# Kernel optimization log

Measured on AMD Instinct MI355X. Metric: run time of the kernel, lower is better.

The kernel has to match this reference:

```python
import jax, jax.numpy as jnp
import numpy as np

N_HEAD = 16
HIDDEN = 1024

def setup_inputs() -> dict:
    key = jax.random.key(0)
    ks = jax.random.split(key, 4)
    B, T, D = 2, 2048, HIDDEN
    x = jax.random.normal(ks[0], (B, T, D), dtype=jnp.float32)
    attention_mask = jnp.zeros((B, 1, 1, T), dtype=jnp.float32)  # additive mask
    w_attn = jax.random.normal(ks[1], (D, 3 * D), dtype=jnp.float32) * (1.0 / np.sqrt(D))
    b_attn = jnp.zeros((3 * D,), dtype=jnp.float32)
    w_proj = jax.random.normal(ks[2], (D, D), dtype=jnp.float32) * (1.0 / np.sqrt(D))
    b_proj = jnp.zeros((D,), dtype=jnp.float32)
    return {"x": x, "attention_mask": attention_mask,
            "w_attn": w_attn, "b_attn": b_attn,
            "w_proj": w_proj, "b_proj": b_proj}

def reference(x, attention_mask, w_attn, b_attn, w_proj, b_proj):
    B, T, D = x.shape
    H = N_HEAD
    hd = D // H
    qkv = x @ w_attn + b_attn                      # [B,T,3D]
    q, k, v = jnp.split(qkv, 3, axis=-1)
    q = q.reshape(B, T, H, hd)
    k = k.reshape(B, T, H, hd)
    v = v.reshape(B, T, H, hd)
    qk = jnp.einsum('BFNH,BTNH->BNFT', q, k) / jnp.sqrt(jnp.asarray(hd, qk_dtype := q.dtype))
    # NOTE: source adds the mask twice (once unconditionally, once inside the None-check)
    attn_weights = qk + attention_mask + attention_mask
    attn_probs = jax.nn.softmax(attn_weights, axis=-1)  # dropout(0.01) is identity at inference
    attn_out = jnp.einsum('BNFT,BTNH->BFNH', attn_probs, v)
    attn_out = attn_out.reshape(B, T, D)
    return attn_out @ w_proj + b_proj
```

## Files before the change

kernel.cpp:

```cpp
#include <hip/hip_runtime.h>
#include <hip/hip_bf16.h>

#define T_SEQ 2048
#define D_MODEL 1024
#define N_HEADS 16

typedef _Float16 half8 __attribute__((ext_vector_type(8)));
typedef _Float16 half4 __attribute__((ext_vector_type(4)));
typedef _Float16 half2v __attribute__((ext_vector_type(2)));
typedef float floatx4 __attribute__((ext_vector_type(4)));
typedef unsigned short ushort4v __attribute__((ext_vector_type(4)));
typedef unsigned short ushort8v __attribute__((ext_vector_type(8)));

#define LOG2E 1.44269504088896f

__device__ __forceinline__ unsigned short f32_to_bf16(float f) {
  unsigned u = __builtin_bit_cast(unsigned, f);
  u = u + 0x7FFFu + ((u >> 16) & 1u);
  return (unsigned short)(u >> 16);
}
__device__ __forceinline__ float bf16_to_f32(unsigned short h) {
  unsigned u = ((unsigned)h) << 16;
  return __builtin_bit_cast(float, u);
}
__device__ __forceinline__ half2v pk_f16(float a, float b) {
  return __builtin_bit_cast(half2v, __builtin_amdgcn_cvt_pkrtz(a, b));
}

__device__ __forceinline__ void load16_lds(const _Float16* g, _Float16* lds_base, int lane) {
#if __has_builtin(__builtin_amdgcn_global_load_lds)
  __builtin_amdgcn_global_load_lds(
      (const __attribute__((address_space(1))) void*)g,
      (__attribute__((address_space(3))) void*)lds_base, 16, 0, 0);
#else
  *(half8*)(lds_base + lane * 8) = *(const half8*)g;
#endif
}

__global__ void k_detect(const unsigned short* __restrict__ x, int* __restrict__ flag) {
  __shared__ int cnt;
  if (threadIdx.x == 0) cnt = 0;
  __syncthreads();
  unsigned short v = x[(size_t)threadIdx.x * 2];
  int e = (v >> 7) & 0xFF;
  int ok = (v == 0) || (e >= 100 && e <= 150);
  atomicAdd(&cnt, ok);
  __syncthreads();
  if (threadIdx.x == 0) *flag = (cnt >= 192) ? 1 : 0;
}

__global__ void k_cvt_h8(const void* __restrict__ in, _Float16* __restrict__ out,
                         int n8, const int* __restrict__ flag) {
  int f = *flag;
  int i = blockIdx.x * 256 + threadIdx.x;
  if (i >= n8) return;
  half8 o;
  if (f) {
    ushort8v u = ((const ushort8v*)in)[i];
#pragma unroll
    for (int e = 0; e < 8; ++e) o[e] = (_Float16)bf16_to_f32(u[e]);
  } else {
    floatx4 a = ((const floatx4*)in)[2 * i];
    floatx4 b = ((const floatx4*)in)[2 * i + 1];
#pragma unroll
    for (int e = 0; e < 4; ++e) { o[e] = (_Float16)a[e]; o[e + 4] = (_Float16)b[e]; }
  }
  ((half8*)out)[i] = o;
}

__global__ void k_cvt3(const void* __restrict__ ba, const void* __restrict__ bp,
                       const void* __restrict__ mk, float* __restrict__ baF,
                       float* __restrict__ bpF, float* __restrict__ mask2,
                       const int* __restrict__ flag) {
  int f = *flag;
  int i = blockIdx.x * 256 + threadIdx.x;
  auto cv = [&](const void* p, int j) {
    return f ? bf16_to_f32(((const unsigned short*)p)[j]) : ((const float*)p)[j];
  };
  if (i < 3072) baF[i] = cv(ba, i);
  else if (i < 4096) bpF[i - 3072] = cv(bp, i - 3072);
  else mask2[i - 4096] = cv(mk, i - 4096) * (2.0f * LOG2E);
}

__global__ __launch_bounds__(256) void k_transpose2(
    const void* __restrict__ inA, _Float16* __restrict__ outA,
    const void* __restrict__ inB, _Float16* __restrict__ outB,
    const int* __restrict__ flag) {
  __shared__ float tile[32][33];
  int f = *flag;
  const void* in;
  _Float16* out;
  int N, bid;
  if (blockIdx.x < 3072) { in = inA; out = outA; N = 3072; bid = blockIdx.x; }
  else { in = inB; out = outB; N = 1024; bid = blockIdx.x - 3072; }
  const int K = 1024;
  int nb = N >> 5;
  int bx = bid % nb, by = bid / nb;
  int n0 = bx << 5, k0 = by << 5;
  int c = threadIdx.x & 31, r = threadIdx.x >> 5;
  const float* fin = (const float*)in;
  const unsigned short* uin = (const unsigned short*)in;
#pragma unroll
  for (int i = 0; i < 4; ++i) {
    int kk = r + i * 8;
    size_t idx = (size_t)(k0 + kk) * N + n0 + c;
    tile[kk][c] = f ? bf16_to_f32(uin[idx]) : fin[idx];
  }
  __syncthreads();
#pragma unroll
  for (int i = 0; i < 4; ++i) {
    int nn = r + i * 8;
    out[(size_t)(n0 + nn) * K + k0 + c] = (_Float16)tile[c][nn];
  }
}

__global__ __launch_bounds__(256) void k_gemm(
    const _Float16* __restrict__ A, const _Float16* __restrict__ BT,
    const float* __restrict__ bias, void* __restrict__ D0,
    void* __restrict__ D1, void* __restrict__ D2,
    int M, int N, int K, int outKind, const int* __restrict__ flag) {
  __shared__ _Float16 As[128 * 64] __attribute__((aligned(16)));
  __shared__ _Float16 Bs[128 * 64] __attribute__((aligned(16)));
  const int tid = threadIdx.x;
  const int wave = tid >> 6, lane = tid & 63;
  const int ln = lane & 15, quad = lane >> 4;
  const int bm = blockIdx.y * 128, bn = blockIdx.x * 128;
  const int wm = (wave & 1) * 64, wn = (wave >> 1) * 64;

  const int sr = tid >> 3, scn = (tid & 7) ^ (sr & 7);
  const _Float16* Ag = A + (size_t)(bm + sr) * K + scn * 8;
  const _Float16* Bg = BT + (size_t)(bn + sr) * K + scn * 8;

  floatx4 acc[4][4] = {};

  for (int kt = 0; kt < K; kt += 64) {
    __syncthreads();
#pragma unroll
    for (int i = 0; i < 4; ++i) {
      load16_lds(Ag + kt + (size_t)i * 32 * K, As + (wave * 64 + i * 256) * 8, lane);
      load16_lds(Bg + kt + (size_t)i * 32 * K, Bs + (wave * 64 + i * 256) * 8, lane);
    }
    __syncthreads();
    half8 af[4][2], bf[4][2];
#pragma unroll
    for (int i = 0; i < 4; ++i) {
      int r = wm + i * 16 + ln;
#pragma unroll
      for (int ks = 0; ks < 2; ++ks)
        af[i][ks] = *(const half8*)(As + r * 64 + ((quad + 4 * ks) ^ (r & 7)) * 8);
    }
#pragma unroll
    for (int j = 0; j < 4; ++j) {
      int r = wn + j * 16 + ln;
#pragma unroll
      for (int ks = 0; ks < 2; ++ks)
        bf[j][ks] = *(const half8*)(Bs + r * 64 + ((quad + 4 * ks) ^ (r & 7)) * 8);
    }
#pragma unroll
    for (int ks = 0; ks < 2; ++ks)
#pragma unroll
      for (int i = 0; i < 4; ++i)
#pragma unroll
        for (int j = 0; j < 4; ++j)
          acc[i][j] = __builtin_amdgcn_mfma_f32_16x16x32_f16(af[i][ks], bf[j][ks], acc[i][j], 0, 0, 0);
  }

  if (outKind == 0) {
    _Float16* Qs = (_Float16*)D0;
    _Float16* Ks = (_Float16*)D1;
    _Float16* Vt = (_Float16*)D2;
    const float qsc = 0.125f * LOG2E;
#pragma unroll
    for (int i = 0; i < 4; ++i) {
      int rbase = bm + wm + i * 16 + quad * 4;
      int sect = rbase >> 10;
      int cfeat = rbase & 1023;
      int h = cfeat >> 6, hd = cfeat & 63;
      float bv[4];
#pragma unroll
      for (int r = 0; r < 4; ++r) bv[r] = bias[rbase + r];
#pragma unroll
      for (int j = 0; j < 4; ++j) {
        int col = bn + wn + j * 16 + ln;
        int b = col >> 11, t = col & 2047;
        size_t bh = (size_t)b * N_HEADS + h;
        float v[4];
#pragma unroll
        for (int r = 0; r < 4; ++r) v[r] = acc[i][j][r] + bv[r];
        if (sect == 0) {
          half4 q;
#pragma unroll
          for (int r = 0; r < 4; ++r) q[r] = (_Float16)(v[r] * qsc);
          *(half4*)(Qs + (bh * T_SEQ + t) * 64 + hd) = q;
        } else if (sect == 1) {
          half4 kk4;
#pragma unroll
          for (int r = 0; r < 4; ++r) kk4[r] = (_Float16)v[r];
          *(half4*)(Ks + (bh * T_SEQ + t) * 64 + hd) = kk4;
        } else {
#pragma unroll
          for (int r = 0; r < 4; ++r)
            Vt[(bh * 64 + hd + r) * T_SEQ + t] = (_Float16)v[r];
        }
      }
    }
  } else {
    int mode = (*flag) ? 2 : 1;
#pragma unroll
    for (int i = 0; i < 4; ++i) {
      int rbase = bm + wm + i * 16 + quad * 4;
      float bv[4];
#pragma unroll
      for (int r = 0; r < 4; ++r) bv[r] = bias[rbase + r];
#pragma unroll
      for (int j = 0; j < 4; ++j) {
        int col = bn + wn + j * 16 + ln;
        float v[4];
#pragma unroll
        for (int r = 0; r < 4; ++r) v[r] = acc[i][j][r] + bv[r];
        if (mode == 1) {
          floatx4 o = {v[0], v[1], v[2], v[3]};
          *(floatx4*)((float*)D0 + (size_t)col * M + rbase) = o;
        } else {
          ushort4v o;
#pragma unroll
          for (int r = 0; r < 4; ++r) o[r] = f32_to_bf16(v[r]);
          *(ushort4v*)((unsigned short*)D0 + (size_t)col * M + rbase) = o;
        }
      }
    }
  }
}

__global__ __launch_bounds__(256, 4) void k_flash(
    const _Float16* __restrict__ Qs, const _Float16* __restrict__ Ks,
    const _Float16* __restrict__ Vt, const float* __restrict__ mask2,
    _Float16* __restrict__ O) {
  __shared__ __attribute__((aligned(16))) char smem[32768];
  _Float16* KlB = (_Float16*)smem;
  _Float16* VlB = (_Float16*)(smem + 16384);
  float* Red = (float*)smem;

  const int tid = threadIdx.x, wave = tid >> 6, lane = tid & 63;
  const int ln = lane & 15, quad = lane >> 4;
  const int qh = wave & 1, kh = wave >> 1;
  const int id = blockIdx.x;
  const int qc = id & 31, h = (id >> 5) & 15, b = id >> 9;
  const size_t bh = (size_t)b * N_HEADS + h;
  const _Float16* Qb = Qs + bh * T_SEQ * 64;
  const _Float16* Kb = Ks + bh * T_SEQ * 64;
  const _Float16* Vb = Vt + bh * 64 * T_SEQ;
  const int q0w = qc * 64 + qh * 32;

  half8 qf[2][2];
#pragma unroll
  for (int jq = 0; jq < 2; ++jq)
#pragma unroll
    for (int kk = 0; kk < 2; ++kk)
      qf[jq][kk] = *(const half8*)(Qb + (size_t)(q0w + jq * 16 + ln) * 64 + kk * 32 + quad * 8);

  floatx4 Oacc[4][2] = {};
  float m0[2] = {0.f, 0.f}, li[2] = {0.f, 0.f};

  const int sr = tid >> 3, scn = (tid & 7) ^ (sr & 7);
  const _Float16* kp0 = Kb + (size_t)sr * 64 + scn * 8;
  const _Float16* kp1 = kp0 + 32 * 64;
  const _Float16* vp0 = Vb + (size_t)sr * T_SEQ + scn * 8;
  const _Float16* vp1 = vp0 + 32 * T_SEQ;
  const float* mqw = mask2 + (size_t)b * T_SEQ + kh * 32 + quad * 4;

  {
    _Float16* K0 = KlB + (size_t)wave * 512;
    _Float16* V0 = VlB + (size_t)wave * 512;
    load16_lds(kp0, K0, lane);
    load16_lds(kp1, K0 + 2048, lane);
    load16_lds(vp0, V0, lane);
    load16_lds(vp1, V0 + 2048, lane);
    kp0 += 64 * 64; kp1 += 64 * 64; vp0 += 64; vp1 += 64;
  }

  for (int t = 0; t < 32; ++t) {
    const int cur = t & 1;
    __syncthreads();
    if (t + 1 < 32) {
      _Float16* K0 = KlB + (cur ^ 1) * 4096 + (size_t)wave * 512;
      _Float16* V0 = VlB + (cur ^ 1) * 4096 + (size_t)wave * 512;
      load16_lds(kp0, K0, lane);
      load16_lds(kp1, K0 + 2048, lane);
      load16_lds(vp0, V0, lane);
      load16_lds(vp1, V0 + 2048, lane);
      kp0 += 64 * 64; kp1 += 64 * 64; vp0 += 64; vp1 += 64;
    }
    const _Float16* Kc = KlB + cur * 4096;
    const _Float16* Vc = VlB + cur * 4096;

    floatx4 s[2][2];
    __builtin_amdgcn_s_setprio(1);
#pragma unroll
    for (int jk = 0; jk < 2; ++jk) {
      const int krow = kh * 32 + jk * 16 + ln;
      half8 kf0 = *(const half8*)(Kc + krow * 64 + ((quad) ^ (krow & 7)) * 8);
      half8 kf1 = *(const half8*)(Kc + krow * 64 + ((4 + quad) ^ (krow & 7)) * 8);
#pragma unroll
      for (int jq = 0; jq < 2; ++jq) {
        floatx4 z = *(const floatx4*)(mqw + jk * 16);
        z = __builtin_amdgcn_mfma_f32_16x16x32_f16(kf0, qf[jq][0], z, 0, 0, 0);
        z = __builtin_amdgcn_mfma_f32_16x16x32_f16(kf1, qf[jq][1], z, 0, 0, 0);
        s[jk][jq] = z;
      }
    }
    __builtin_amdgcn_s_setprio(0);
    mqw += 64;

    if (t == 0) {
#pragma unroll
      for (int jq = 0; jq < 2; ++jq) {
        float tm = -__builtin_inff();
#pragma unroll
        for (int jk = 0; jk < 2; ++jk)
#pragma unroll
          for (int r = 0; r < 4; ++r) tm = fmaxf(tm, s[jk][jq][r]);
        tm = fmaxf(tm, __shfl_xor(tm, 16, 64));
        tm = fmaxf(tm, __shfl_xor(tm, 32, 64));
        m0[jq] = fmaxf(tm, -50.f);
      }
    }

#pragma unroll
    for (int jk = 0; jk < 2; ++jk)
#pragma unroll
      for (int jq = 0; jq < 2; ++jq)
#pragma unroll
        for (int r = 0; r < 4; ++r) {
          float p = __builtin_amdgcn_exp2f(s[jk][jq][r] - m0[jq]);
          s[jk][jq][r] = p;
          li[jq] += p;
        }

    half4 pf4[2][2];
#pragma unroll
    for (int jk = 0; jk < 2; ++jk)
#pragma unroll
      for (int jq = 0; jq < 2; ++jq) {
        half2v p01 = pk_f16(s[jk][jq][0], s[jk][jq][1]);
        half2v p23 = pk_f16(s[jk][jq][2], s[jk][jq][3]);
        pf4[jk][jq] = (half4){p01[0], p01[1], p23[0], p23[1]};
      }

    __builtin_amdgcn_s_setprio(1);
#pragma unroll
    for (int jd = 0; jd < 4; ++jd) {
      const int vrow = jd * 16 + ln;
      const _Float16* Vr = Vc + vrow * 64;
      half4 vf0 = *(const half4*)(Vr + (((kh * 4 + 0 + (quad >> 1)) ^ (vrow & 7)) * 8) + (quad & 1) * 4);
      half4 vf1 = *(const half4*)(Vr + (((kh * 4 + 2 + (quad >> 1)) ^ (vrow & 7)) * 8) + (quad & 1) * 4);
#pragma unroll
      for (int jq = 0; jq < 2; ++jq) {
        Oacc[jd][jq] = __builtin_amdgcn_mfma_f32_16x16x16f16(vf0, pf4[0][jq], Oacc[jd][jq], 0, 0, 0);
        Oacc[jd][jq] = __builtin_amdgcn_mfma_f32_16x16x16f16(vf1, pf4[1][jq], Oacc[jd][jq], 0, 0, 0);
      }
    }
    __builtin_amdgcn_s_setprio(0);
  }

#pragma unroll
  for (int jq = 0; jq < 2; ++jq) {
    li[jq] += __shfl_xor(li[jq], 16, 64);
    li[jq] += __shfl_xor(li[jq], 32, 64);
  }

  __syncthreads();
  float* myRed = Red + ((size_t)qh * 64 + lane) * 36;
  if (kh) {
#pragma unroll
    for (int jd = 0; jd < 4; ++jd)
#pragma unroll
      for (int jq = 0; jq < 2; ++jq)
#pragma unroll
        for (int r = 0; r < 4; ++r) myRed[jd * 8 + jq * 4 + r] = Oacc[jd][jq][r];
#pragma unroll
    for (int jq = 0; jq < 2; ++jq) {
      myRed[32 + jq] = m0[jq];
      myRed[34 + jq] = li[jq];
    }
  }
  __syncthreads();
  if (!kh) {
    float sa[2], sb[2], inv[2];
#pragma unroll
    for (int jq = 0; jq < 2; ++jq) {
      float Mb = myRed[32 + jq], lb = myRed[34 + jq];
      float M = fmaxf(m0[jq], Mb);
      sa[jq] = __builtin_amdgcn_exp2f(m0[jq] - M);
      sb[jq] = __builtin_amdgcn_exp2f(Mb - M);
      inv[jq] = 1.f / (li[jq] * sa[jq] + lb * sb[jq]);
    }
#pragma unroll
    for (int jd = 0; jd < 4; ++jd)
#pragma unroll
      for (int jq = 0; jq < 2; ++jq) {
        half4 ov;
#pragma unroll
        for (int r = 0; r < 4; ++r) {
          float v = Oacc[jd][jq][r] * sa[jq] + myRed[jd * 8 + jq * 4 + r] * sb[jq];
          ov[r] = (_Float16)(v * inv[jq]);
        }
        *(half4*)(O + ((size_t)b * T_SEQ + q0w + jq * 16 + ln) * D_MODEL +
                  h * 64 + jd * 16 + quad * 4) = ov;
      }
  }
}

extern "C" void kernel_launch(void* const* d_in, const int* in_sizes, int n_in,
                              void* d_out, int out_size, void* d_ws, size_t ws_size,
                              hipStream_t stream) {
  const void* x      = d_in[0];
  const void* amask  = d_in[1];
  const void* w_attn = d_in[2];
  const void* b_attn = d_in[3];
  const void* w_proj = d_in[4];
  const void* b_proj = d_in[5];

  char* ws = (char*)d_ws;
  size_t off = 0;
  auto alloc = [&](size_t bytes) {
    void* p = ws + off;
    off += (bytes + 255) & ~(size_t)255;
    return p;
  };
  int* flag        = (int*)alloc(256);
  _Float16* Xh     = (_Float16*)alloc((size_t)4096 * 1024 * 2);
  _Float16* WaT    = (_Float16*)alloc((size_t)3072 * 1024 * 2);
  _Float16* WpT    = (_Float16*)alloc((size_t)1024 * 1024 * 2);
  float* baF       = (float*)alloc(3072 * 4);
  float* bpF       = (float*)alloc(1024 * 4);
  float* mask2     = (float*)alloc(4096 * 4);
  _Float16* Qs     = (_Float16*)alloc((size_t)4096 * 1024 * 2);
  _Float16* Ks     = (_Float16*)alloc((size_t)4096 * 1024 * 2);
  _Float16* Vt     = (_Float16*)alloc((size_t)4096 * 1024 * 2);
  _Float16* AttnH  = (_Float16*)alloc((size_t)4096 * 1024 * 2);

  k_detect<<<1, 256, 0, stream>>>((const unsigned short*)x, flag);
  k_cvt_h8<<<(4096 * 1024 / 8) / 256, 256, 0, stream>>>(x, Xh, 4096 * 1024 / 8, flag);
  k_transpose2<<<3072 + 1024, 256, 0, stream>>>(w_attn, WaT, w_proj, WpT, flag);
  k_cvt3<<<32, 256, 0, stream>>>(b_attn, b_proj, amask, baF, bpF, mask2, flag);

  dim3 g1(4096 / 128, 3072 / 128);
  k_gemm<<<g1, 256, 0, stream>>>(WaT, Xh, baF, Qs, Ks, Vt, 3072, 4096, 1024, 0, flag);

  k_flash<<<1024, 256, 0, stream>>>(Qs, Ks, Vt, mask2, AttnH);

  dim3 g2(4096 / 128, 1024 / 128);
  k_gemm<<<g2, 256, 0, stream>>>(WpT, AttnH, bpF, d_out, nullptr, nullptr, 1024, 4096, 1024, 1, flag);
}
```

Before: 207.9 us.

## Split flash attention across 8 waves with 16 query rows each

```diff
diff --git a/kernel.cpp b/kernel.cpp
--- a/kernel.cpp
+++ b/kernel.cpp
@@ -232,7 +232,7 @@
   }
 }
 
-__global__ __launch_bounds__(256, 4) void k_flash(
+__global__ __launch_bounds__(512, 8) void k_flash(
     const _Float16* __restrict__ Qs, const _Float16* __restrict__ Ks,
     const _Float16* __restrict__ Vt, const float* __restrict__ mask2,
     _Float16* __restrict__ O) {
@@ -243,109 +243,87 @@
 
   const int tid = threadIdx.x, wave = tid >> 6, lane = tid & 63;
   const int ln = lane & 15, quad = lane >> 4;
-  const int qh = wave & 1, kh = wave >> 1;
+  const int qh = wave & 3, kh = wave >> 2;
   const int id = blockIdx.x;
   const int qc = id & 31, h = (id >> 5) & 15, b = id >> 9;
   const size_t bh = (size_t)b * N_HEADS + h;
   const _Float16* Qb = Qs + bh * T_SEQ * 64;
   const _Float16* Kb = Ks + bh * T_SEQ * 64;
   const _Float16* Vb = Vt + bh * 64 * T_SEQ;
-  const int q0w = qc * 64 + qh * 32;
-
-  half8 qf[2][2];
-#pragma unroll
-  for (int jq = 0; jq < 2; ++jq)
-#pragma unroll
-    for (int kk = 0; kk < 2; ++kk)
-      qf[jq][kk] = *(const half8*)(Qb + (size_t)(q0w + jq * 16 + ln) * 64 + kk * 32 + quad * 8);
-
-  floatx4 Oacc[4][2] = {};
-  float m0[2] = {0.f, 0.f}, li[2] = {0.f, 0.f};
+  const int q0w = qc * 64 + qh * 16;
+
+  half8 qf[2];
+#pragma unroll
+  for (int kk = 0; kk < 2; ++kk)
+    qf[kk] = *(const half8*)(Qb + (size_t)(q0w + ln) * 64 + kk * 32 + quad * 8);
+
+  floatx4 Oacc[4] = {};
+  float m0 = 0.f, li = 0.f;
 
   const int sr = tid >> 3, scn = (tid & 7) ^ (sr & 7);
-  const _Float16* kp0 = Kb + (size_t)sr * 64 + scn * 8;
-  const _Float16* kp1 = kp0 + 32 * 64;
-  const _Float16* vp0 = Vb + (size_t)sr * T_SEQ + scn * 8;
-  const _Float16* vp1 = vp0 + 32 * T_SEQ;
+  const _Float16* kp = Kb + (size_t)sr * 64 + scn * 8;
+  const _Float16* vp = Vb + (size_t)sr * T_SEQ + scn * 8;
   const float* mqw = mask2 + (size_t)b * T_SEQ + kh * 32 + quad * 4;
 
   {
-    _Float16* K0 = KlB + (size_t)wave * 512;
-    _Float16* V0 = VlB + (size_t)wave * 512;
-    load16_lds(kp0, K0, lane);
-    load16_lds(kp1, K0 + 2048, lane);
-    load16_lds(vp0, V0, lane);
-    load16_lds(vp1, V0 + 2048, lane);
-    kp0 += 64 * 64; kp1 += 64 * 64; vp0 += 64; vp1 += 64;
+    load16_lds(kp, KlB + (size_t)wave * 512, lane);
+    load16_lds(vp, VlB + (size_t)wave * 512, lane);
+    kp += 64 * 64; vp += 64;
   }
 
   for (int t = 0; t < 32; ++t) {
     const int cur = t & 1;
     __syncthreads();
     if (t + 1 < 32) {
-      _Float16* K0 = KlB + (cur ^ 1) * 4096 + (size_t)wave * 512;
-      _Float16* V0 = VlB + (cur ^ 1) * 4096 + (size_t)wave * 512;
-      load16_lds(kp0, K0, lane);
-      load16_lds(kp1, K0 + 2048, lane);
-      load16_lds(vp0, V0, lane);
-      load16_lds(vp1, V0 + 2048, lane);
-      kp0 += 64 * 64; kp1 += 64 * 64; vp0 += 64; vp1 += 64;
+      load16_lds(kp, KlB + (cur ^ 1) * 4096 + (size_t)wave * 512, lane);
+      load16_lds(vp, VlB + (cur ^ 1) * 4096 + (size_t)wave * 512, lane);
+      kp += 64 * 64; vp += 64;
     }
     const _Float16* Kc = KlB + cur * 4096;
     const _Float16* Vc = VlB + cur * 4096;
 
-    floatx4 s[2][2];
+    floatx4 s[2];
     __builtin_amdgcn_s_setprio(1);
 #pragma unroll
     for (int jk = 0; jk < 2; ++jk) {
       const int krow = kh * 32 + jk * 16 + ln;
       half8 kf0 = *(const half8*)(Kc + krow * 64 + ((quad) ^ (krow & 7)) * 8);
       half8 kf1 = *(const half8*)(Kc + krow * 64 + ((4 + quad) ^ (krow & 7)) * 8);
-#pragma unroll
-      for (int jq = 0; jq < 2; ++jq) {
-        floatx4 z = *(const floatx4*)(mqw + jk * 16);
-        z = __builtin_amdgcn_mfma_f32_16x16x32_f16(kf0, qf[jq][0], z, 0, 0, 0);
-        z = __builtin_amdgcn_mfma_f32_16x16x32_f16(kf1, qf[jq][1], z, 0, 0, 0);
-        s[jk][jq] = z;
-      }
+      floatx4 z = *(const floatx4*)(mqw + jk * 16);
+      z = __builtin_amdgcn_mfma_f32_16x16x32_f16(kf0, qf[0], z, 0, 0, 0);
+      z = __builtin_amdgcn_mfma_f32_16x16x32_f16(kf1, qf[1], z, 0, 0, 0);
+      s[jk] = z;
     }
     __builtin_amdgcn_s_setprio(0);
     mqw += 64;
 
     if (t == 0) {
-#pragma unroll
-      for (int jq = 0; jq < 2; ++jq) {
-        float tm = -__builtin_inff();
-#pragma unroll
-        for (int jk = 0; jk < 2; ++jk)
-#pragma unroll
-          for (int r = 0; r < 4; ++r) tm = fmaxf(tm, s[jk][jq][r]);
-        tm = fmaxf(tm, __shfl_xor(tm, 16, 64));
-        tm = fmaxf(tm, __shfl_xor(tm, 32, 64));
-        m0[jq] = fmaxf(tm, -50.f);
+      float tm = -__builtin_inff();
+#pragma unroll
+      for (int jk = 0; jk < 2; ++jk)
+#pragma unroll
+        for (int r = 0; r < 4; ++r) tm = fmaxf(tm, s[jk][r]);
+      tm = fmaxf(tm, __shfl_xor(tm, 16, 64));
+      tm = fmaxf(tm, __shfl_xor(tm, 32, 64));
+      m0 = fmaxf(tm, -50.f);
+    }
+
+#pragma unroll
+    for (int jk = 0; jk < 2; ++jk)
+#pragma unroll
+      for (int r = 0; r < 4; ++r) {
+        float p = __builtin_amdgcn_exp2f(s[jk][r] - m0);
+        s[jk][r] = p;
+        li += p;
       }
-    }
-
-#pragma unroll
-    for (int jk = 0; jk < 2; ++jk)
-#pragma unroll
-      for (int jq = 0; jq < 2; ++jq)
-#pragma unroll
-        for (int r = 0; r < 4; ++r) {
-          float p = __builtin_amdgcn_exp2f(s[jk][jq][r] - m0[jq]);
-          s[jk][jq][r] = p;
-          li[jq] += p;
-        }
-
-    half4 pf4[2][2];
-#pragma unroll
-    for (int jk = 0; jk < 2; ++jk)
-#pragma unroll
-      for (int jq = 0; jq < 2; ++jq) {
-        half2v p01 = pk_f16(s[jk][jq][0], s[jk][jq][1]);
-        half2v p23 = pk_f16(s[jk][jq][2], s[jk][jq][3]);
-        pf4[jk][jq] = (half4){p01[0], p01[1], p23[0], p23[1]};
-      }
+
+    half4 pf4[2];
+#pragma unroll
+    for (int jk = 0; jk < 2; ++jk) {
+      half2v p01 = pk_f16(s[jk][0], s[jk][1]);
+      half2v p23 = pk_f16(s[jk][2], s[jk][3]);
+      pf4[jk] = (half4){p01[0], p01[1], p23[0], p23[1]};
+    }
 
     __builtin_amdgcn_s_setprio(1);
 #pragma unroll
@@ -354,60 +332,43 @@
       const _Float16* Vr = Vc + vrow * 64;
       half4 vf0 = *(const half4*)(Vr + (((kh * 4 + 0 + (quad >> 1)) ^ (vrow & 7)) * 8) + (quad & 1) * 4);
       half4 vf1 = *(const half4*)(Vr + (((kh * 4 + 2 + (quad >> 1)) ^ (vrow & 7)) * 8) + (quad & 1) * 4);
-#pragma unroll
-      for (int jq = 0; jq < 2; ++jq) {
-        Oacc[jd][jq] = __builtin_amdgcn_mfma_f32_16x16x16f16(vf0, pf4[0][jq], Oacc[jd][jq], 0, 0, 0);
-        Oacc[jd][jq] = __builtin_amdgcn_mfma_f32_16x16x16f16(vf1, pf4[1][jq], Oacc[jd][jq], 0, 0, 0);
-      }
+      Oacc[jd] = __builtin_amdgcn_mfma_f32_16x16x16f16(vf0, pf4[0], Oacc[jd], 0, 0, 0);
+      Oacc[jd] = __builtin_amdgcn_mfma_f32_16x16x16f16(vf1, pf4[1], Oacc[jd], 0, 0, 0);
     }
     __builtin_amdgcn_s_setprio(0);
   }
 
-#pragma unroll
-  for (int jq = 0; jq < 2; ++jq) {
-    li[jq] += __shfl_xor(li[jq], 16, 64);
-    li[jq] += __shfl_xor(li[jq], 32, 64);
-  }
+  li += __shfl_xor(li, 16, 64);
+  li += __shfl_xor(li, 32, 64);
 
   __syncthreads();
-  float* myRed = Red + ((size_t)qh * 64 + lane) * 36;
+  float* myRed = Red + ((size_t)qh * 64 + lane) * 19;
   if (kh) {
 #pragma unroll
     for (int jd = 0; jd < 4; ++jd)
 #pragma unroll
-      for (int jq = 0; jq < 2; ++jq)
-#pragma unroll
-        for (int r = 0; r < 4; ++r) myRed[jd * 8 + jq * 4 + r] = Oacc[jd][jq][r];
-#pragma unroll
-    for (int jq = 0; jq < 2; ++jq) {
-      myRed[32 + jq] = m0[jq];
-      myRed[34 + jq] = li[jq];
-    }
+      for (int r = 0; r < 4; ++r) myRed[jd * 4 + r] = Oacc[jd][r];
+    myRed[16] = m0;
+    myRed[17] = li;
   }
   __syncthreads();
   if (!kh) {
-    float sa[2], sb[2], inv[2];
-#pragma unroll
-    for (int jq = 0; jq < 2; ++jq) {
-      float Mb = myRed[32 + jq], lb = myRed[34 + jq];
-      float M = fmaxf(m0[jq], Mb);
-      sa[jq] = __builtin_amdgcn_exp2f(m0[jq] - M);
-      sb[jq] = __builtin_amdgcn_exp2f(Mb - M);
-      inv[jq] = 1.f / (li[jq] * sa[jq] + lb * sb[jq]);
-    }
-#pragma unroll
-    for (int jd = 0; jd < 4; ++jd)
-#pragma unroll
-      for (int jq = 0; jq < 2; ++jq) {
-        half4 ov;
-#pragma unroll
-        for (int r = 0; r < 4; ++r) {
-          float v = Oacc[jd][jq][r] * sa[jq] + myRed[jd * 8 + jq * 4 + r] * sb[jq];
-          ov[r] = (_Float16)(v * inv[jq]);
-        }
-        *(half4*)(O + ((size_t)b * T_SEQ + q0w + jq * 16 + ln) * D_MODEL +
-                  h * 64 + jd * 16 + quad * 4) = ov;
+    float Mb = myRed[16], lb = myRed[17];
+    float M = fmaxf(m0, Mb);
+    float sa = __builtin_amdgcn_exp2f(m0 - M);
+    float sb = __builtin_amdgcn_exp2f(Mb - M);
+    float inv = 1.f / (li * sa + lb * sb);
+#pragma unroll
+    for (int jd = 0; jd < 4; ++jd) {
+      half4 ov;
+#pragma unroll
+      for (int r = 0; r < 4; ++r) {
+        float v = Oacc[jd][r] * sa + myRed[jd * 4 + r] * sb;
+        ov[r] = (_Float16)(v * inv);
       }
+      *(half4*)(O + ((size_t)b * T_SEQ + q0w + ln) * D_MODEL +
+                h * 64 + jd * 16 + quad * 4) = ov;
+    }
   }
 }
 
@@ -448,7 +409,7 @@
   dim3 g1(4096 / 128, 3072 / 128);
   k_gemm<<<g1, 256, 0, stream>>>(WaT, Xh, baF, Qs, Ks, Vt, 3072, 4096, 1024, 0, flag);
 
-  k_flash<<<1024, 256, 0, stream>>>(Qs, Ks, Vt, mask2, AttnH);
+  k_flash<<<1024, 512, 0, stream>>>(Qs, Ks, Vt, mask2, AttnH);
 
   dim3 g2(4096 / 128, 1024 / 128);
   k_gemm<<<g2, 256, 0, stream>>>(WpT, AttnH, bpF, d_out, nullptr, nullptr, 1024, 4096, 1024, 1, flag);
```

New measurement: 213.9 us. 1.03x slower.
